# Performance work log

Measured on AMD Instinct MI355X. Metric: run time of the kernel, lower is better.

## Reference

```python
import jax, jax.numpy as jnp
import numpy as np

N = 32000
E = 512000
IN_C = 16
OUT_C = 16
EDGE_DIM = 8
HID = 32


def setup_inputs() -> dict:
    key = jax.random.key(0)
    ks = jax.random.split(key, 8)
    x = jax.random.normal(ks[0], (N, IN_C), dtype=jnp.float32)
    edge_index = jax.random.randint(ks[1], (2, E), 0, N, dtype=jnp.int32)
    pseudo = jax.random.uniform(ks[2], (E, EDGE_DIM), dtype=jnp.float32)
    W1 = jax.random.normal(ks[3], (EDGE_DIM, HID), dtype=jnp.float32) * (1.0 / np.sqrt(EDGE_DIM))
    b1 = jnp.zeros((HID,), dtype=jnp.float32)
    W2 = jax.random.normal(ks[4], (HID, IN_C * OUT_C), dtype=jnp.float32) * (1.0 / np.sqrt(HID))
    b2 = jnp.zeros((IN_C * OUT_C,), dtype=jnp.float32)
    root = jax.random.normal(ks[5], (IN_C, OUT_C), dtype=jnp.float32) * (1.0 / np.sqrt(IN_C))
    bias = jnp.zeros((OUT_C,), dtype=jnp.float32)
    return {"x": x, "edge_index": edge_index, "pseudo": pseudo,
            "W1": W1, "b1": b1, "W2": W2, "b2": b2,
            "root": root, "bias": bias}


def reference(x, edge_index, pseudo, W1, b1, W2, b2, root, bias):
    row, col = edge_index[0], edge_index[1]
    # edge MLP h_Theta: [E, edge_dim] -> [E, in*out]
    h = jax.nn.relu(pseudo @ W1 + b1)
    w = (h @ W2 + b2).reshape(-1, IN_C, OUT_C)  # [E, in, out]
    # gather source features, per-edge matmul: [E, in] x [E, in, out] -> [E, out]
    msg = jnp.einsum('ei,eio->eo', x[col], w)
    # scatter-add messages to destination nodes (aggr='add')
    out = jax.ops.segment_sum(msg, row, num_segments=N)
    # root transform + bias
    out = out + x @ root + bias
    return out
```

## Files before the change

### kernel.cpp

```cpp
#include <hip/hip_runtime.h>
#include <stdint.h>
#include <limits.h>

#define IN_C   16
#define OUT_C  16
#define EDGE_DIM 8
#define HID    32
#define HSTR   20
#define XSTR   20
#define MAXDEG 48
#define FEPB   128

typedef __attribute__((ext_vector_type(8))) short short8v;
typedef __attribute__((ext_vector_type(4))) float f32x4;

__device__ __forceinline__ uint32_t pack_bf16(float a, float b) {
    union { float f; uint32_t u; } ua, ub;
    ua.f = a; ub.f = b;
    uint32_t lo = (ua.u + 0x7FFFu + ((ua.u >> 16) & 1u)) >> 16;
    uint32_t hi = (ub.u + 0x7FFFu + ((ub.u >> 16) & 1u)) >> 16;
    return (lo & 0xFFFFu) | (hi << 16);
}

__global__ __launch_bounds__(256) void nnconv_prep(
    const float* __restrict__ W2, uint4* __restrict__ W2p,
    const float* __restrict__ b2, float* __restrict__ b2t,
    int* __restrict__ zero_base, int n_zero_ints)
{
    int bid = blockIdx.x;
    if (bid < 4) {
        int idx = bid * 256 + threadIdx.x;
        int ci = idx >> 6, l = idx & 63;
        int o = l & 15, g = l >> 4;
        uint32_t u[4];
        #pragma unroll
        for (int v = 0; v < 4; ++v) {
            int k0 = g * 8 + 2 * v;
            u[v] = pack_bf16(W2[(size_t)k0 * 256 + ci * 16 + o],
                             W2[(size_t)(k0 + 1) * 256 + ci * 16 + o]);
        }
        W2p[idx] = make_uint4(u[0], u[1], u[2], u[3]);
        return;
    }
    if (bid == 4) {
        int t = threadIdx.x;
        b2t[t] = b2[(t & 15) * 16 + (t >> 4)];
        return;
    }
    int t = (bid - 5) * 256 + threadIdx.x;
    int stride = (gridDim.x - 5) * 256;
    for (int i = t; i < n_zero_ints; i += stride)
        zero_base[i] = 0;
}

__global__ __launch_bounds__(256, 2) void nnconv_fused1(
    const float* __restrict__ pseudo, const int* __restrict__ eidx,
    const float* __restrict__ x,
    const float* __restrict__ W1, const float* __restrict__ b1,
    const uint4* __restrict__ W2p, const float* __restrict__ b2t,
    int* __restrict__ cur, float* __restrict__ ovf,
    uint32_t* __restrict__ msgu, int n_edges)
{
    __shared__ uint32_t Hl[FEPB * HSTR];
    __shared__ float    xl[FEPB * XSTR];
    __shared__ uint4    Wl[1024];

    int t  = threadIdx.x;
    int e0 = blockIdx.x * FEPB;
    int e  = e0 + t;
    bool valid = e < n_edges;
    int lane = t & 63, w = t >> 6;
    int o = lane & 15, g = lane >> 4;

    int row = 0;
    float p[EDGE_DIM];
    {
        float4* xd = reinterpret_cast<float4*>(&xl[t * XSTR]);
        if (valid) {
            row = eidx[e];
            int c = eidx[n_edges + e];
            const float4* xp = reinterpret_cast<const float4*>(x + (size_t)c * IN_C);
            xd[0] = xp[0]; xd[1] = xp[1]; xd[2] = xp[2]; xd[3] = xp[3];
            const float4* pp = reinterpret_cast<const float4*>(pseudo + (size_t)e * EDGE_DIM);
            float4 p0 = pp[0], p1 = pp[1];
            p[0]=p0.x; p[1]=p0.y; p[2]=p0.z; p[3]=p0.w;
            p[4]=p1.x; p[5]=p1.y; p[6]=p1.z; p[7]=p1.w;
        } else {
            float4 z = make_float4(0.f, 0.f, 0.f, 0.f);
            xd[0] = z; xd[1] = z; xd[2] = z; xd[3] = z;
            #pragma unroll
            for (int k = 0; k < EDGE_DIM; ++k) p[k] = 0.f;
        }
    }
    float b2v[16];
    {
        const float4* bp = reinterpret_cast<const float4*>(b2t + o * 16);
        #pragma unroll
        for (int c4 = 0; c4 < 4; ++c4) {
            float4 bv = bp[c4];
            b2v[c4*4+0] = bv.x; b2v[c4*4+1] = bv.y;
            b2v[c4*4+2] = bv.z; b2v[c4*4+3] = bv.w;
        }
    }

    for (int ch = 0; ch < 4; ++ch) {
        uint4 c0 = W2p[lane + (ch * 4 + 0) * 64];
        uint4 c1 = W2p[lane + (ch * 4 + 1) * 64];
        uint4 c2 = W2p[lane + (ch * 4 + 2) * 64];
        uint4 c3 = W2p[lane + (ch * 4 + 3) * 64];
        Wl[lane + (ch * 4 + 0) * 64] = c0;
        Wl[lane + (ch * 4 + 1) * 64] = c1;
        Wl[lane + (ch * 4 + 2) * 64] = c2;
        Wl[lane + (ch * 4 + 3) * 64] = c3;
    }

    {
        float h[HID];
        #pragma unroll
        for (int j = 0; j < HID; ++j) h[j] = b1[j];
        #pragma unroll
        for (int k = 0; k < EDGE_DIM; ++k) {
            float pk = p[k];
            const float* wr = W1 + k * HID;
            #pragma unroll
            for (int j = 0; j < HID; ++j)
                h[j] = fmaf(pk, wr[j], h[j]);
        }
        uint32_t hw[16];
        #pragma unroll
        for (int v = 0; v < 16; ++v) {
            float a0 = h[2*v]   > 0.f ? h[2*v]   : 0.f;
            float a1 = h[2*v+1] > 0.f ? h[2*v+1] : 0.f;
            hw[v] = valid ? pack_bf16(a0, a1) : 0u;
        }
        uint4* hp = reinterpret_cast<uint4*>(&Hl[t * HSTR]);
        hp[0] = make_uint4(hw[0],  hw[1],  hw[2],  hw[3]);
        hp[1] = make_uint4(hw[4],  hw[5],  hw[6],  hw[7]);
        hp[2] = make_uint4(hw[8],  hw[9],  hw[10], hw[11]);
        hp[3] = make_uint4(hw[12], hw[13], hw[14], hw[15]);
    }

    int slv = INT_MIN;
    if (valid) {
        int rank = atomicAdd(&cur[row], 1);
        slv = (rank < MAXDEG) ? (row * MAXDEG + rank) : (-row - 1);
    }

    int ebase = w * 64;

    #pragma unroll
    for (int q = 0; q < 4; ++q) {
        short8v A = *reinterpret_cast<const short8v*>(
            &Hl[(size_t)(ebase + q * 16 + o) * HSTR + g * 4]);
        float macc[4] = {0.f, 0.f, 0.f, 0.f};
        #pragma unroll
        for (int cq = 0; cq < 4; ++cq) {
            short8v Bf[4];
            #pragma unroll
            for (int j = 0; j < 4; ++j)
                Bf[j] = *reinterpret_cast<const short8v*>(&Wl[(cq * 4 + j) * 64 + lane]);
            f32x4 C[4];
            #pragma unroll
            for (int j = 0; j < 4; ++j) {
                float bb = b2v[cq * 4 + j];
                C[j] = __builtin_amdgcn_mfma_f32_16x16x32_bf16(
                    A, Bf[j], (f32x4){bb, bb, bb, bb}, 0, 0, 0);
            }
            #pragma unroll
            for (int r = 0; r < 4; ++r) {
                int el = ebase + q * 16 + g * 4 + r;
                float4 xa = *reinterpret_cast<const float4*>(&xl[el * XSTR + cq * 4]);
                float m = macc[r];
                m = fmaf(xa.x, C[0][r], m); m = fmaf(xa.y, C[1][r], m);
                m = fmaf(xa.z, C[2][r], m); m = fmaf(xa.w, C[3][r], m);
                macc[r] = m;
            }
        }
        #pragma unroll
        for (int r = 0; r < 4; ++r) {
            int el = q * 16 + g * 4 + r;
            int sl = __shfl(slv, el, 64);
            float other = __shfl_xor(macc[r], 1, 64);
            if (sl >= 0) {
                if (!(o & 1)) {
                    uint32_t dw = pack_bf16(macc[r], other);
                    msgu[(size_t)sl * 8 + (o >> 1)] = dw;
                }
            } else if (sl != INT_MIN) {
                atomicAdd(&ovf[(size_t)(-sl - 1) * OUT_C + o], macc[r]);
            }
        }
    }
}

__global__ __launch_bounds__(256) void nnconv_gather1(
    const uint32_t* __restrict__ msgu, const int* __restrict__ cur,
    const float* __restrict__ ovf, const float* __restrict__ x,
    const float* __restrict__ root, const float* __restrict__ bias,
    float* __restrict__ out, int n_nodes)
{
    int wave = threadIdx.x >> 6, lane = threadIdx.x & 63;
    int n = blockIdx.x * 4 + wave;
    if (n >= n_nodes) return;
    int group = lane >> 4, o = lane & 15;
    int craw = cur[n];
    int cntn = craw > MAXDEG ? MAXDEG : craw;
    size_t s = (size_t)n * MAXDEG;
    float acc = 0.f;
    int half = o & 1;
    int dwi = o >> 1;
    for (int k = group; k < cntn; k += 4) {
        uint32_t u = msgu[(s + k) * 8 + dwi];
        uint32_t h16 = half ? (u & 0xFFFF0000u) : (u << 16);
        union { uint32_t u; float f; } cv; cv.u = h16;
        acc += cv.f;
    }
    acc += __shfl_xor(acc, 16, 64);
    acc += __shfl_xor(acc, 32, 64);
    if (group == 0) {
        float r = bias[o];
        if (craw > MAXDEG) r += ovf[(size_t)n * OUT_C + o];
        const float* xr = x + (size_t)n * IN_C;
        #pragma unroll
        for (int i = 0; i < IN_C; ++i)
            r = fmaf(xr[i], root[i * OUT_C + o], r);
        out[n * OUT_C + o] = r + acc;
    }
}


__global__ __launch_bounds__(256) void nnconv_init_out(
    const float* __restrict__ x, const float* __restrict__ root,
    const float* __restrict__ bias, float* __restrict__ out, int n_nodes)
{
    int t = blockIdx.x * blockDim.x + threadIdx.x;
    if (t >= n_nodes * OUT_C) return;
    int n = t >> 4, o = t & 15;
    float acc = bias[o];
    #pragma unroll
    for (int i = 0; i < IN_C; ++i)
        acc = fmaf(x[n * IN_C + i], root[i * OUT_C + o], acc);
    out[t] = acc;
}

__global__ __launch_bounds__(256) void nnconv_edge_atomic(
    const float* __restrict__ x, const int* __restrict__ edge_index,
    const float* __restrict__ pseudo,
    const float* __restrict__ W1, const float* __restrict__ b1,
    const float* __restrict__ W2, const float* __restrict__ b2,
    float* __restrict__ out, int n_edges)
{
    int e = blockIdx.x * blockDim.x + threadIdx.x;
    if (e >= n_edges) return;
    int row = edge_index[e];
    int col = edge_index[n_edges + e];
    float p[EDGE_DIM];
    const float4* pp = reinterpret_cast<const float4*>(pseudo + (size_t)e * EDGE_DIM);
    float4 p0 = pp[0], p1 = pp[1];
    p[0]=p0.x; p[1]=p0.y; p[2]=p0.z; p[3]=p0.w;
    p[4]=p1.x; p[5]=p1.y; p[6]=p1.z; p[7]=p1.w;
    float h[HID];
    #pragma unroll
    for (int j = 0; j < HID; ++j) {
        float a = b1[j];
        #pragma unroll
        for (int k = 0; k < EDGE_DIM; ++k)
            a = fmaf(p[k], W1[k * HID + j], a);
        h[j] = a > 0.f ? a : 0.f;
    }
    float xg[IN_C];
    const float4* xp = reinterpret_cast<const float4*>(x + (size_t)col * IN_C);
    #pragma unroll
    for (int q = 0; q < 4; ++q) {
        float4 v = xp[q];
        xg[q*4+0]=v.x; xg[q*4+1]=v.y; xg[q*4+2]=v.z; xg[q*4+3]=v.w;
    }
    float m[OUT_C];
    #pragma unroll
    for (int o = 0; o < OUT_C; ++o) m[o] = 0.f;
    for (int i = 0; i < IN_C; ++i) {
        float wv[OUT_C];
        const float* b2r = b2 + i * OUT_C;
        #pragma unroll
        for (int o = 0; o < OUT_C; ++o) wv[o] = b2r[o];
        #pragma unroll
        for (int j = 0; j < HID; ++j) {
            float hj = h[j];
            const float* wr = W2 + j * (IN_C * OUT_C) + i * OUT_C;
            #pragma unroll
            for (int o = 0; o < OUT_C; ++o)
                wv[o] = fmaf(hj, wr[o], wv[o]);
        }
        float xi = xg[i];
        #pragma unroll
        for (int o = 0; o < OUT_C; ++o)
            m[o] = fmaf(xi, wv[o], m[o]);
    }
    float* op = out + (size_t)row * OUT_C;
    #pragma unroll
    for (int o = 0; o < OUT_C; ++o)
        atomicAdd(op + o, m[o]);
}


extern "C" void kernel_launch(void* const* d_in, const int* in_sizes, int n_in,
                              void* d_out, int out_size, void* d_ws, size_t ws_size,
                              hipStream_t stream) {
    const float* x      = (const float*)d_in[0];
    const int*   eidx   = (const int*)  d_in[1];
    const float* pseudo = (const float*)d_in[2];
    const float* W1     = (const float*)d_in[3];
    const float* b1     = (const float*)d_in[4];
    const float* W2     = (const float*)d_in[5];
    const float* b2     = (const float*)d_in[6];
    const float* root   = (const float*)d_in[7];
    const float* bias   = (const float*)d_in[8];
    float* out = (float*)d_out;

    int n_nodes = in_sizes[0] / IN_C;
    int n_edges = in_sizes[1] / 2;
    int eblocks256 = (n_edges + 255) / 256;
    char* wsp = (char*)d_ws;

    {
        int* cur1  = (int*)wsp;
        float* ovf = (float*)(cur1 + n_nodes);
        size_t off = sizeof(int) * (size_t)n_nodes + sizeof(float) * (size_t)n_nodes * OUT_C;
        off = (off + 255) & ~(size_t)255;
        uint4* W2p = (uint4*)(wsp + off);
        off += sizeof(uint4) * 1024;
        float* b2t = (float*)(wsp + off);
        off += sizeof(float) * 256;
        off = (off + 255) & ~(size_t)255;
        uint32_t* msgu = (uint32_t*)(wsp + off);
        size_t need = off + sizeof(uint32_t) * (size_t)n_nodes * MAXDEG * 8;

        if (ws_size >= need) {
            int n_zero_ints = n_nodes + n_nodes * OUT_C;
            nnconv_prep<<<5 + 64, 256, 0, stream>>>(W2, W2p, b2, b2t, cur1, n_zero_ints);
            nnconv_fused1<<<(n_edges + FEPB - 1) / FEPB, FEPB, 0, stream>>>(
                pseudo, eidx, x, W1, b1, W2p, b2t, cur1, ovf, msgu, n_edges);
            nnconv_gather1<<<(n_nodes + 3) / 4, 256, 0, stream>>>(
                msgu, cur1, ovf, x, root, bias, out, n_nodes);
            return;
        }
    }

    nnconv_init_out<<<(n_nodes * OUT_C + 255) / 256, 256, 0, stream>>>(
        x, root, bias, out, n_nodes);
    nnconv_edge_atomic<<<eblocks256, 256, 0, stream>>>(
        x, eidx, pseudo, W1, b1, W2, b2, out, n_edges);
}
```

Baseline: 78.82 us.

## Decouple edge bucketing from message compute using edge-id lists and overflow pass

Edge messages are now written contiguously in edge order instead of scattered into per-node slots. Alternate blocks of the main kernel only bin edges by destination, recording edge ids per node, with an overflow list for nodes past MAXDEG. The gather kernel then reads messages indirectly through the id list, and a new small kernel atomically adds the overflow edges. This takes the row atomic off the compute blocks' critical path and drops zeroing of the dense overflow buffer, at the cost of an extra indirection in the gather, an extra launch, and a fixed overflow capacity that silently drops edges beyond it.

```diff
diff --git a/kernel.cpp b/kernel.cpp
--- a/kernel.cpp
+++ b/kernel.cpp
@@ -1,6 +1,5 @@
 #include <hip/hip_runtime.h>
 #include <stdint.h>
-#include <limits.h>
 
 #define IN_C   16
 #define OUT_C  16
@@ -10,6 +9,7 @@
 #define XSTR   20
 #define MAXDEG 48
 #define FEPB   128
+#define OVFCAP 65536
 
 typedef __attribute__((ext_vector_type(8))) short short8v;
 typedef __attribute__((ext_vector_type(4))) float f32x4;
@@ -53,31 +53,47 @@
         zero_base[i] = 0;
 }
 
-__global__ __launch_bounds__(256, 2) void nnconv_fused1(
+__global__ __launch_bounds__(256, 2) void nnconv_main(
     const float* __restrict__ pseudo, const int* __restrict__ eidx,
     const float* __restrict__ x,
     const float* __restrict__ W1, const float* __restrict__ b1,
     const uint4* __restrict__ W2p, const float* __restrict__ b2t,
-    int* __restrict__ cur, float* __restrict__ ovf,
+    int* __restrict__ cur, int* __restrict__ eid,
+    int* __restrict__ ovfeid, int* __restrict__ novf,
     uint32_t* __restrict__ msgu, int n_edges)
 {
     __shared__ uint32_t Hl[FEPB * HSTR];
     __shared__ float    xl[FEPB * XSTR];
     __shared__ uint4    Wl[1024];
 
-    int t  = threadIdx.x;
-    int e0 = blockIdx.x * FEPB;
+    int t   = threadIdx.x;
+    int bid = blockIdx.x;
+
+    if (bid & 1) {
+        int e2 = (bid >> 1) * FEPB + t;
+        if (e2 < n_edges) {
+            int r = eidx[e2];
+            int rank = atomicAdd(&cur[r], 1);
+            if (rank < MAXDEG) {
+                eid[(size_t)r * MAXDEG + rank] = e2;
+            } else {
+                int pos = atomicAdd(novf, 1);
+                if (pos < OVFCAP) ovfeid[pos] = e2;
+            }
+        }
+        return;
+    }
+
+    int e0 = (bid >> 1) * FEPB;
     int e  = e0 + t;
     bool valid = e < n_edges;
     int lane = t & 63, w = t >> 6;
     int o = lane & 15, g = lane >> 4;
 
-    int row = 0;
     float p[EDGE_DIM];
     {
         float4* xd = reinterpret_cast<float4*>(&xl[t * XSTR]);
         if (valid) {
-            row = eidx[e];
             int c = eidx[n_edges + e];
             const float4* xp = reinterpret_cast<const float4*>(x + (size_t)c * IN_C);
             xd[0] = xp[0]; xd[1] = xp[1]; xd[2] = xp[2]; xd[3] = xp[3];
@@ -140,12 +156,6 @@
         hp[3] = make_uint4(hw[12], hw[13], hw[14], hw[15]);
     }
 
-    int slv = INT_MIN;
-    if (valid) {
-        int rank = atomicAdd(&cur[row], 1);
-        slv = (rank < MAXDEG) ? (row * MAXDEG + rank) : (-row - 1);
-    }
-
     int ebase = w * 64;
 
     #pragma unroll
@@ -178,16 +188,11 @@
         }
         #pragma unroll
         for (int r = 0; r < 4; ++r) {
-            int el = q * 16 + g * 4 + r;
-            int sl = __shfl(slv, el, 64);
+            int el = ebase + q * 16 + g * 4 + r;
             float other = __shfl_xor(macc[r], 1, 64);
-            if (sl >= 0) {
-                if (!(o & 1)) {
-                    uint32_t dw = pack_bf16(macc[r], other);
-                    msgu[(size_t)sl * 8 + (o >> 1)] = dw;
-                }
-            } else if (sl != INT_MIN) {
-                atomicAdd(&ovf[(size_t)(-sl - 1) * OUT_C + o], macc[r]);
+            if (!(o & 1) && (e0 + el) < n_edges) {
+                uint32_t dw = pack_bf16(macc[r], other);
+                msgu[(size_t)(e0 + el) * 8 + (o >> 1)] = dw;
             }
         }
     }
@@ -195,7 +200,7 @@
 
 __global__ __launch_bounds__(256) void nnconv_gather1(
     const uint32_t* __restrict__ msgu, const int* __restrict__ cur,
-    const float* __restrict__ ovf, const float* __restrict__ x,
+    const int* __restrict__ eid, const float* __restrict__ x,
     const float* __restrict__ root, const float* __restrict__ bias,
     float* __restrict__ out, int n_nodes)
 {
@@ -205,12 +210,13 @@
     int group = lane >> 4, o = lane & 15;
     int craw = cur[n];
     int cntn = craw > MAXDEG ? MAXDEG : craw;
-    size_t s = (size_t)n * MAXDEG;
+    const int* el = eid + (size_t)n * MAXDEG;
     float acc = 0.f;
     int half = o & 1;
     int dwi = o >> 1;
     for (int k = group; k < cntn; k += 4) {
-        uint32_t u = msgu[(s + k) * 8 + dwi];
+        int e = el[k];
+        uint32_t u = msgu[(size_t)e * 8 + dwi];
         uint32_t h16 = half ? (u & 0xFFFF0000u) : (u << 16);
         union { uint32_t u; float f; } cv; cv.u = h16;
         acc += cv.f;
@@ -219,12 +225,29 @@
     acc += __shfl_xor(acc, 32, 64);
     if (group == 0) {
         float r = bias[o];
-        if (craw > MAXDEG) r += ovf[(size_t)n * OUT_C + o];
         const float* xr = x + (size_t)n * IN_C;
         #pragma unroll
         for (int i = 0; i < IN_C; ++i)
             r = fmaf(xr[i], root[i * OUT_C + o], r);
         out[n * OUT_C + o] = r + acc;
+    }
+}
+
+__global__ __launch_bounds__(256) void nnconv_ovf(
+    const uint32_t* __restrict__ msgu, const int* __restrict__ ovfeid,
+    const int* __restrict__ novf, const int* __restrict__ eidx,
+    float* __restrict__ out, int n_edges)
+{
+    int cnt = *novf; if (cnt > OVFCAP) cnt = OVFCAP;
+    int total = cnt * OUT_C;
+    for (int i = blockIdx.x * 256 + threadIdx.x; i < total; i += gridDim.x * 256) {
+        int idx = i >> 4, o = i & 15;
+        int e = ovfeid[idx];
+        int row = eidx[e];
+        uint32_t u = msgu[(size_t)e * 8 + (o >> 1)];
+        uint32_t h16 = (o & 1) ? (u & 0xFFFF0000u) : (u << 16);
+        union { uint32_t u; float f; } cv; cv.u = h16;
+        atomicAdd(&out[(size_t)row * OUT_C + o], cv.f);
     }
 }
 
@@ -319,29 +342,37 @@
 
     int n_nodes = in_sizes[0] / IN_C;
     int n_edges = in_sizes[1] / 2;
+    int eblocks128 = (n_edges + FEPB - 1) / FEPB;
     int eblocks256 = (n_edges + 255) / 256;
+    size_t Epad = (size_t)eblocks128 * FEPB;
     char* wsp = (char*)d_ws;
 
     {
-        int* cur1  = (int*)wsp;
-        float* ovf = (float*)(cur1 + n_nodes);
-        size_t off = sizeof(int) * (size_t)n_nodes + sizeof(float) * (size_t)n_nodes * OUT_C;
+        int* cur1   = (int*)wsp;
+        int* novf   = cur1 + n_nodes;
+        int* ovfeid = novf + 64;
+        size_t off = sizeof(int) * ((size_t)n_nodes + 64 + OVFCAP);
         off = (off + 255) & ~(size_t)255;
         uint4* W2p = (uint4*)(wsp + off);
         off += sizeof(uint4) * 1024;
         float* b2t = (float*)(wsp + off);
         off += sizeof(float) * 256;
         off = (off + 255) & ~(size_t)255;
+        int* eid = (int*)(wsp + off);
+        off += sizeof(int) * (size_t)n_nodes * MAXDEG;
+        off = (off + 255) & ~(size_t)255;
         uint32_t* msgu = (uint32_t*)(wsp + off);
-        size_t need = off + sizeof(uint32_t) * (size_t)n_nodes * MAXDEG * 8;
+        size_t need = off + sizeof(uint32_t) * Epad * 8;
 
         if (ws_size >= need) {
-            int n_zero_ints = n_nodes + n_nodes * OUT_C;
-            nnconv_prep<<<5 + 64, 256, 0, stream>>>(W2, W2p, b2, b2t, cur1, n_zero_ints);
-            nnconv_fused1<<<(n_edges + FEPB - 1) / FEPB, FEPB, 0, stream>>>(
-                pseudo, eidx, x, W1, b1, W2p, b2t, cur1, ovf, msgu, n_edges);
+            int n_zero_ints = n_nodes + 64;
+            nnconv_prep<<<5 + 32, 256, 0, stream>>>(W2, W2p, b2, b2t, cur1, n_zero_ints);
+            nnconv_main<<<2 * eblocks128, FEPB, 0, stream>>>(
+                pseudo, eidx, x, W1, b1, W2p, b2t,
+                cur1, eid, ovfeid, novf, msgu, n_edges);
             nnconv_gather1<<<(n_nodes + 3) / 4, 256, 0, stream>>>(
-                msgu, cur1, ovf, x, root, bias, out, n_nodes);
+                msgu, cur1, eid, x, root, bias, out, n_nodes);
+            nnconv_ovf<<<8, 256, 0, stream>>>(msgu, ovfeid, novf, eidx, out, n_edges);
             return;
         }
     }
```

After: 121.4 us. 1.54x slower.

## Replace global atomic slot assignment with chunked LDS histogram plus scan CSR layout

Applied to the files above, without the earlier changes.

Replaces the per-edge global atomicAdd on node counters (fixed MAXDEG slots plus an overflow atomic path) with a two-pass counting sort. Per-chunk LDS histograms give each edge a local rank, and a scan kernel builds chunk bases, giving compact CSR offsets for messages. This removes global atomic contention and the overflow path, and packs messages densely so the gather reads contiguous memory. The cost is two extra kernels, a K×RPAD chunkbase table of global traffic, and a hard limit of n_nodes ≤ 32768 and at most 65535 edges per destination per chunk.

```diff
diff --git a/kernel.cpp b/kernel.cpp
--- a/kernel.cpp
+++ b/kernel.cpp
@@ -1,6 +1,5 @@
 #include <hip/hip_runtime.h>
 #include <stdint.h>
-#include <limits.h>
 
 #define IN_C   16
 #define OUT_C  16
@@ -8,8 +7,10 @@
 #define HID    32
 #define HSTR   20
 #define XSTR   20
-#define MAXDEG 48
 #define FEPB   128
+#define CHUNK  4096
+#define RPAD   32768
+#define HDW    (RPAD/2)
 
 typedef __attribute__((ext_vector_type(8))) short short8v;
 typedef __attribute__((ext_vector_type(4))) float f32x4;
@@ -22,35 +23,94 @@
     return (lo & 0xFFFFu) | (hi << 16);
 }
 
-__global__ __launch_bounds__(256) void nnconv_prep(
+__global__ __launch_bounds__(256) void nnconv_rank(
+    const int* __restrict__ eidx, uint16_t* __restrict__ lrank16,
+    uint32_t* __restrict__ histg,
     const float* __restrict__ W2, uint4* __restrict__ W2p,
     const float* __restrict__ b2, float* __restrict__ b2t,
-    int* __restrict__ zero_base, int n_zero_ints)
-{
-    int bid = blockIdx.x;
-    if (bid < 4) {
-        int idx = bid * 256 + threadIdx.x;
-        int ci = idx >> 6, l = idx & 63;
-        int o = l & 15, g = l >> 4;
-        uint32_t u[4];
-        #pragma unroll
-        for (int v = 0; v < 4; ++v) {
-            int k0 = g * 8 + 2 * v;
-            u[v] = pack_bf16(W2[(size_t)k0 * 256 + ci * 16 + o],
-                             W2[(size_t)(k0 + 1) * 256 + ci * 16 + o]);
-        }
-        W2p[idx] = make_uint4(u[0], u[1], u[2], u[3]);
+    int* __restrict__ total, int n_edges, int K)
+{
+    __shared__ uint32_t hist[HDW];
+    int bid = blockIdx.x, t = threadIdx.x;
+
+    if (bid >= K) {
+        if (bid < K + 4) {
+            int idx = (bid - K) * 256 + t;
+            int ci = idx >> 6, l = idx & 63;
+            int o = l & 15, g = l >> 4;
+            uint32_t u[4];
+            #pragma unroll
+            for (int v = 0; v < 4; ++v) {
+                int k0 = g * 8 + 2 * v;
+                u[v] = pack_bf16(W2[(size_t)k0 * 256 + ci * 16 + o],
+                                 W2[(size_t)(k0 + 1) * 256 + ci * 16 + o]);
+            }
+            W2p[idx] = make_uint4(u[0], u[1], u[2], u[3]);
+        } else {
+            b2t[t] = b2[(t & 15) * 16 + (t >> 4)];
+            if (t == 0) *total = 0;
+        }
         return;
     }
-    if (bid == 4) {
-        int t = threadIdx.x;
-        b2t[t] = b2[(t & 15) * 16 + (t >> 4)];
-        return;
-    }
-    int t = (bid - 5) * 256 + threadIdx.x;
-    int stride = (gridDim.x - 5) * 256;
-    for (int i = t; i < n_zero_ints; i += stride)
-        zero_base[i] = 0;
+
+    for (int i = t; i < HDW; i += 256) hist[i] = 0;
+    __syncthreads();
+
+    int ebase = bid * CHUNK;
+    #pragma unroll
+    for (int it = 0; it < CHUNK / 256; ++it) {
+        int e = ebase + it * 256 + t;
+        if (e < n_edges) {
+            int r = eidx[e];
+            uint32_t inc = (r & 1) ? 0x10000u : 1u;
+            uint32_t old = atomicAdd(&hist[r >> 1], inc);
+            uint32_t lr = (r & 1) ? (old >> 16) : (old & 0xFFFFu);
+            lrank16[e] = (uint16_t)lr;
+        }
+    }
+    __syncthreads();
+
+    uint32_t* hg = histg + (size_t)bid * HDW;
+    for (int i = t; i < HDW; i += 256) hg[i] = hist[i];
+}
+
+__global__ __launch_bounds__(256) void nnconv_scan(
+    const uint32_t* __restrict__ histg, uint32_t* __restrict__ chunkbase,
+    int* __restrict__ baseArr, int* __restrict__ cntArr,
+    int* __restrict__ total, int K)
+{
+    int rr = blockIdx.x * 256 + threadIdx.x;
+    int lane = threadIdx.x & 63;
+    uint32_t sumlo = 0, sumhi = 0;
+    for (int k = 0; k < K; ++k) {
+        uint32_t u = histg[(size_t)k * HDW + rr];
+        sumlo += u & 0xFFFFu;
+        sumhi += u >> 16;
+    }
+    int comb = (int)(sumlo + sumhi);
+    int s = comb;
+    #pragma unroll
+    for (int d = 1; d < 64; d <<= 1) {
+        int v = __shfl_up(s, d, 64);
+        if (lane >= d) s += v;
+    }
+    int wsum = __shfl(s, 63, 64);
+    int wbase = 0;
+    if (lane == 63) wbase = atomicAdd(total, wsum);
+    wbase = __shfl(wbase, 63, 64);
+    int myex = wbase + s - comb;
+    int r0 = 2 * rr, r1 = 2 * rr + 1;
+    int baselo = myex, basehi = myex + (int)sumlo;
+    baseArr[r0] = baselo; baseArr[r1] = basehi;
+    cntArr[r0]  = (int)sumlo; cntArr[r1] = (int)sumhi;
+    uint32_t lo = (uint32_t)baselo, hi = (uint32_t)basehi;
+    for (int k = 0; k < K; ++k) {
+        uint32_t u = histg[(size_t)k * HDW + rr];
+        chunkbase[(size_t)k * RPAD + r0] = lo;
+        chunkbase[(size_t)k * RPAD + r1] = hi;
+        lo += u & 0xFFFFu;
+        hi += u >> 16;
+    }
 }
 
 __global__ __launch_bounds__(256, 2) void nnconv_fused1(
@@ -58,7 +118,7 @@
     const float* __restrict__ x,
     const float* __restrict__ W1, const float* __restrict__ b1,
     const uint4* __restrict__ W2p, const float* __restrict__ b2t,
-    int* __restrict__ cur, float* __restrict__ ovf,
+    const uint32_t* __restrict__ chunkbase, const uint16_t* __restrict__ lrank16,
     uint32_t* __restrict__ msgu, int n_edges)
 {
     __shared__ uint32_t Hl[FEPB * HSTR];
@@ -71,13 +131,15 @@
     bool valid = e < n_edges;
     int lane = t & 63, w = t >> 6;
     int o = lane & 15, g = lane >> 4;
-
-    int row = 0;
+    int kch = e0 / CHUNK;
+
+    int slv = -1;
     float p[EDGE_DIM];
     {
         float4* xd = reinterpret_cast<float4*>(&xl[t * XSTR]);
         if (valid) {
-            row = eidx[e];
+            int r = eidx[e];
+            slv = (int)chunkbase[(size_t)kch * RPAD + r] + (int)lrank16[e];
             int c = eidx[n_edges + e];
             const float4* xp = reinterpret_cast<const float4*>(x + (size_t)c * IN_C);
             xd[0] = xp[0]; xd[1] = xp[1]; xd[2] = xp[2]; xd[3] = xp[3];
@@ -140,12 +202,6 @@
         hp[3] = make_uint4(hw[12], hw[13], hw[14], hw[15]);
     }
 
-    int slv = INT_MIN;
-    if (valid) {
-        int rank = atomicAdd(&cur[row], 1);
-        slv = (rank < MAXDEG) ? (row * MAXDEG + rank) : (-row - 1);
-    }
-
     int ebase = w * 64;
 
     #pragma unroll
@@ -181,21 +237,17 @@
             int el = q * 16 + g * 4 + r;
             int sl = __shfl(slv, el, 64);
             float other = __shfl_xor(macc[r], 1, 64);
-            if (sl >= 0) {
-                if (!(o & 1)) {
-                    uint32_t dw = pack_bf16(macc[r], other);
-                    msgu[(size_t)sl * 8 + (o >> 1)] = dw;
-                }
-            } else if (sl != INT_MIN) {
-                atomicAdd(&ovf[(size_t)(-sl - 1) * OUT_C + o], macc[r]);
+            if (sl >= 0 && !(o & 1)) {
+                uint32_t dw = pack_bf16(macc[r], other);
+                msgu[(size_t)sl * 8 + (o >> 1)] = dw;
             }
         }
     }
 }
 
 __global__ __launch_bounds__(256) void nnconv_gather1(
-    const uint32_t* __restrict__ msgu, const int* __restrict__ cur,
-    const float* __restrict__ ovf, const float* __restrict__ x,
+    const uint32_t* __restrict__ msgu, const int* __restrict__ baseArr,
+    const int* __restrict__ cntArr, const float* __restrict__ x,
     const float* __restrict__ root, const float* __restrict__ bias,
     float* __restrict__ out, int n_nodes)
 {
@@ -203,9 +255,8 @@
     int n = blockIdx.x * 4 + wave;
     if (n >= n_nodes) return;
     int group = lane >> 4, o = lane & 15;
-    int craw = cur[n];
-    int cntn = craw > MAXDEG ? MAXDEG : craw;
-    size_t s = (size_t)n * MAXDEG;
+    int cntn = cntArr[n];
+    size_t s = (size_t)baseArr[n];
     float acc = 0.f;
     int half = o & 1;
     int dwi = o >> 1;
@@ -219,7 +270,6 @@
     acc += __shfl_xor(acc, 32, 64);
     if (group == 0) {
         float r = bias[o];
-        if (craw > MAXDEG) r += ovf[(size_t)n * OUT_C + o];
         const float* xr = x + (size_t)n * IN_C;
         #pragma unroll
         for (int i = 0; i < IN_C; ++i)
@@ -319,29 +369,41 @@
 
     int n_nodes = in_sizes[0] / IN_C;
     int n_edges = in_sizes[1] / 2;
+    int eblocks128 = (n_edges + FEPB - 1) / FEPB;
     int eblocks256 = (n_edges + 255) / 256;
+    int K = (n_edges + CHUNK - 1) / CHUNK;
     char* wsp = (char*)d_ws;
 
-    {
-        int* cur1  = (int*)wsp;
-        float* ovf = (float*)(cur1 + n_nodes);
-        size_t off = sizeof(int) * (size_t)n_nodes + sizeof(float) * (size_t)n_nodes * OUT_C;
+    if (n_nodes <= RPAD) {
+        int* baseArr = (int*)wsp;
+        int* cntArr  = baseArr + RPAD;
+        int* total   = cntArr + RPAD;
+        size_t off = sizeof(int) * (size_t)(2 * RPAD + 64);
         off = (off + 255) & ~(size_t)255;
         uint4* W2p = (uint4*)(wsp + off);
         off += sizeof(uint4) * 1024;
         float* b2t = (float*)(wsp + off);
         off += sizeof(float) * 256;
         off = (off + 255) & ~(size_t)255;
+        uint16_t* lrank16 = (uint16_t*)(wsp + off);
+        off += sizeof(uint16_t) * (size_t)eblocks128 * FEPB;
+        off = (off + 255) & ~(size_t)255;
+        uint32_t* histg = (uint32_t*)(wsp + off);
+        off += sizeof(uint32_t) * (size_t)K * HDW;
+        uint32_t* chunkbase = (uint32_t*)(wsp + off);
+        off += sizeof(uint32_t) * (size_t)K * RPAD;
         uint32_t* msgu = (uint32_t*)(wsp + off);
-        size_t need = off + sizeof(uint32_t) * (size_t)n_nodes * MAXDEG * 8;
+        size_t need = off + sizeof(uint32_t) * (size_t)n_edges * 8;
 
         if (ws_size >= need) {
-            int n_zero_ints = n_nodes + n_nodes * OUT_C;
-            nnconv_prep<<<5 + 64, 256, 0, stream>>>(W2, W2p, b2, b2t, cur1, n_zero_ints);
-            nnconv_fused1<<<(n_edges + FEPB - 1) / FEPB, FEPB, 0, stream>>>(
-                pseudo, eidx, x, W1, b1, W2p, b2t, cur1, ovf, msgu, n_edges);
+            nnconv_rank<<<K + 5, 256, 0, stream>>>(
+                eidx, lrank16, histg, W2, W2p, b2, b2t, total, n_edges, K);
+            nnconv_scan<<<HDW / 256, 256, 0, stream>>>(
+                histg, chunkbase, baseArr, cntArr, total, K);
+            nnconv_fused1<<<eblocks128, FEPB, 0, stream>>>(
+                pseudo, eidx, x, W1, b1, W2p, b2t, chunkbase, lrank16, msgu, n_edges);
             nnconv_gather1<<<(n_nodes + 3) / 4, 256, 0, stream>>>(
-                msgu, cur1, ovf, x, root, bias, out, n_nodes);
+                msgu, baseArr, cntArr, x, root, bias, out, n_nodes);
             return;
         }
     }
```

Result: slower. 121.3 us (+53.9%).
